# Optimization experiments

Measured on AMD Instinct MI355X. Metric: run time of the kernel, lower is better.

The kernel has to match this reference:

```python
import math
import jax, jax.numpy as jnp
import numpy as np

B, S, G, CMAX, T = 128, 256, 8, 6, 32
E, NH, L, Z = 64, 4, 2, 3
DFF = 4 * E


def _conv1d(x, w, b, pad):
    # x: [N, C, T], w: [O, I, K] -> [N, O, T]
    y = jax.lax.conv_general_dilated(x, w, (1,), [(pad, pad)], dimension_numbers=('NCH', 'OIH', 'NCH'))
    return y + b[None, :, None]


def _layernorm(x, g, b, eps=1e-5):
    m = jnp.mean(x, -1, keepdims=True)
    v = jnp.mean((x - m) ** 2, -1, keepdims=True)
    return (x - m) * jax.lax.rsqrt(v + eps) * g + b


def _pos_encoding(seq_len, dim):
    pos = jnp.arange(seq_len, dtype=jnp.float32)[:, None]
    div = jnp.exp(jnp.arange(0, dim, 2, dtype=jnp.float32) * (-math.log(10000.0) / dim))
    pe = jnp.zeros((seq_len, dim), dtype=jnp.float32)
    pe = pe.at[:, 0::2].set(jnp.sin(pos * div)).at[:, 1::2].set(jnp.cos(pos * div))
    return pe


def setup_inputs() -> dict:
    key = jax.random.key(0)
    ks = iter(jax.random.split(key, 48))
    def nrm(shape, s=0.05):
        return (jax.random.normal(next(ks), shape) * s).astype(jnp.float32)
    inp = {}
    inp['waveforms'] = jax.random.normal(next(ks), (B, S, CMAX, T), dtype=jnp.float32)
    inp['shank_ids'] = jax.random.randint(next(ks), (B, S), 0, G)
    lengths = jax.random.randint(next(ks), (B,), S // 2, S + 1)
    inp['mask'] = jnp.arange(S)[None, :] >= lengths[:, None]  # True = padded
    inp['conv1_w'] = nrm((G, 32, CMAX, 5), 0.1)
    inp['conv1_b'] = jnp.zeros((G, 32), jnp.float32)
    inp['conv2_w'] = nrm((G, E, 32, 3), 0.1)
    inp['conv2_b'] = jnp.zeros((G, E), jnp.float32)
    inp['shank_emb'] = nrm((G, E), 0.02)
    inp['in_proj_w'] = nrm((L, 3 * E, E))
    inp['in_proj_b'] = jnp.zeros((L, 3 * E), jnp.float32)
    inp['out_proj_w'] = nrm((L, E, E))
    inp['out_proj_b'] = jnp.zeros((L, E), jnp.float32)
    inp['ln1_g'] = jnp.ones((L, E), jnp.float32)
    inp['ln1_b'] = jnp.zeros((L, E), jnp.float32)
    inp['ff1_w'] = nrm((L, DFF, E))
    inp['ff1_b'] = jnp.zeros((L, DFF), jnp.float32)
    inp['ff2_w'] = nrm((L, E, DFF))
    inp['ff2_b'] = jnp.zeros((L, E), jnp.float32)
    inp['ln2_g'] = jnp.ones((L, E), jnp.float32)
    inp['ln2_b'] = jnp.zeros((L, E), jnp.float32)
    inp['cls_w1'] = nrm((E, E)); inp['cls_b1'] = jnp.zeros((E,), jnp.float32)
    inp['cls_w2'] = nrm((Z, E)); inp['cls_b2'] = jnp.zeros((Z,), jnp.float32)
    inp['mu_w1'] = nrm((Z, E, E)); inp['mu_b1'] = jnp.zeros((Z, E), jnp.float32)
    inp['mu_w2'] = nrm((Z, 2, E)); inp['mu_b2'] = jnp.zeros((Z, 2), jnp.float32)
    inp['ls_w1'] = nrm((Z, E, E)); inp['ls_b1'] = jnp.zeros((Z, E), jnp.float32)
    inp['ls_w2'] = nrm((Z, 2, E)); inp['ls_b2'] = jnp.zeros((Z, 2), jnp.float32)
    inp['d_w1'] = nrm((E, E)); inp['d_b1'] = jnp.zeros((E,), jnp.float32)
    inp['d_w2'] = nrm((1, E)); inp['d_b2'] = jnp.zeros((1,), jnp.float32)
    return inp


def reference(waveforms, shank_ids, mask, conv1_w, conv1_b, conv2_w, conv2_b, shank_emb,
              in_proj_w, in_proj_b, out_proj_w, out_proj_b, ln1_g, ln1_b,
              ff1_w, ff1_b, ff2_w, ff2_b, ln2_g, ln2_b,
              cls_w1, cls_b1, cls_w2, cls_b2, mu_w1, mu_b1, mu_w2, mu_b2,
              ls_w1, ls_b1, ls_w2, ls_b2, d_w1, d_b1, d_w2, d_b2):
    b, s, c, t = waveforms.shape
    e = shank_emb.shape[1]
    g = shank_emb.shape[0]
    x = waveforms.reshape(b * s, c, t)
    # per-shank conv encoders (MoE-style dispatch); loop over fixed small expert set
    embs = []
    for i in range(g):
        h1 = jax.nn.relu(_conv1d(x, conv1_w[i], conv1_b[i], 2))   # [N,32,T]
        h2 = jax.nn.relu(_conv1d(h1, conv2_w[i], conv2_b[i], 1))  # [N,E,T]
        embs.append(h2.mean(-1))                                  # AdaptiveAvgPool1d(1)
    emb_all = jnp.stack(embs, axis=1)                             # [N,G,E]
    sid = shank_ids.reshape(-1)
    emb = jnp.take_along_axis(emb_all, sid[:, None, None], axis=1)[:, 0]  # [N,E]
    active = (~mask).reshape(-1)
    emb = jnp.where(active[:, None], emb, 0.0).reshape(b, s, e)   # masked slots stay zero
    emb = emb + shank_emb[shank_ids] + _pos_encoding(s, e)[None]
    # post-norm transformer encoder, relu FFN, eval mode (dropout off)
    dh = e // NH
    key_bias = jnp.where(mask, -1e9, 0.0).astype(emb.dtype)[:, None, None, :]  # [B,1,1,S]
    h = emb
    for l in range(in_proj_w.shape[0]):
        qkv = h @ in_proj_w[l].T + in_proj_b[l]
        q, k, v = jnp.split(qkv, 3, axis=-1)
        q = q.reshape(b, s, NH, dh)
        k = k.reshape(b, s, NH, dh)
        v = v.reshape(b, s, NH, dh)
        scores = jnp.einsum('bqhd,bkhd->bhqk', q, k) / math.sqrt(dh) + key_bias
        attn = jax.nn.softmax(scores, axis=-1)
        o = jnp.einsum('bhqk,bkhd->bqhd', attn, v).reshape(b, s, e)
        o = o @ out_proj_w[l].T + out_proj_b[l]
        h = _layernorm(h + o, ln1_g[l], ln1_b[l])
        ff = jax.nn.relu(h @ ff1_w[l].T + ff1_b[l]) @ ff2_w[l].T + ff2_b[l]
        h = _layernorm(h + ff, ln2_g[l], ln2_b[l])
    am = active.reshape(b, s, 1).astype(h.dtype)
    pooled = (h * am).sum(1) / (am.sum(1) + 1e-8)                 # masked mean pool [B,E]
    cls_logits = jax.nn.relu(pooled @ cls_w1.T + cls_b1) @ cls_w2.T + cls_b2
    hz = jax.nn.relu(jnp.einsum('be,zfe->zbf', pooled, mu_w1) + mu_b1[:, None])
    mus = jnp.einsum('zbf,zof->bzo', hz, mu_w2) + mu_b2[None]     # [B,Z,2]
    hs = jax.nn.relu(jnp.einsum('be,zfe->zbf', pooled, ls_w1) + ls_b1[:, None])
    sigmas = jnp.exp(jnp.einsum('zbf,zof->bzo', hs, ls_w2) + ls_b2[None])  # [B,Z,2]
    d_pred = jax.nn.sigmoid(jax.nn.relu(pooled @ d_w1.T + d_b1) @ d_w2.T + d_b2)
    return jnp.concatenate([cls_logits, mus.reshape(b, -1), sigmas.reshape(b, -1), d_pred], axis=-1)
```

## Files before the change

kernel.cpp:

```cpp
#include <hip/hip_runtime.h>
#include <math.h>


typedef short bf16x8 __attribute__((ext_vector_type(8)));
typedef float f32x4 __attribute__((ext_vector_type(4)));

__device__ __forceinline__ unsigned short f2bf(float f) {
  unsigned u = __float_as_uint(f);
  u += 0x7fffu + ((u >> 16) & 1u);
  return (unsigned short)(u >> 16);
}

__device__ __forceinline__ bf16x8 ldfrag(const unsigned short* p) {
  return *reinterpret_cast<const bf16x8*>(p);
}

__device__ __forceinline__ bool is_masked(const void* mask_, int flag, int idx) {
  return flag ? (((const unsigned char*)mask_)[idx] != 0)
              : (((const int*)mask_)[idx] != 0);
}

__global__ __launch_bounds__(256) void prep_weights_kernel(
    const float* __restrict__ in_proj_w, const float* __restrict__ out_proj_w,
    const float* __restrict__ ff1_w, const float* __restrict__ ff2_w,
    const float* __restrict__ w1_, const float* __restrict__ w2_,
    unsigned short* __restrict__ wb) {
  int i = blockIdx.x * 256 + threadIdx.x;
  if (i < 24576) {
    int rem = i % 12288, row = rem / 64;
    float v = in_proj_w[i];
    if (row < 64) v *= 0.25f;
    wb[i] = f2bf(v);
  } else if (i < 32768) {
    wb[i] = f2bf(out_proj_w[i - 24576]);
  } else if (i < 65536) {
    wb[i] = f2bf(ff1_w[i - 32768]);
  } else if (i < 98304) {
    wb[i] = f2bf(ff2_w[i - 65536]);
  } else if (i < 108544) {
    int j = i - 98304;
    int g = j / 1280, rem = j % 1280;
    int k = rem >> 8, rest = rem & 255, oc = rest >> 3, ic = rest & 7;
    wb[i] = (ic < 6) ? f2bf(w1_[g * 960 + oc * 30 + ic * 5 + k]) : 0;
  } else if (i < 169984) {
    int j = i - 108544;
    int g = j / 7680, rem = j % 7680;
    int k = rem / 2560, rest = rem % 2560, e = rest / 40, ic = rest % 40;
    wb[i] = (ic < 32) ? f2bf(w2_[g * 6144 + e * 96 + ic * 3 + k]) : 0;
  }
}

__global__ void detect_mask_kernel(const unsigned int* __restrict__ mw,
                                   int* __restrict__ flag, int* __restrict__ counts,
                                   int* __restrict__ lens) {
  __shared__ int sh;
  if (threadIdx.x == 0) sh = 0;
  __syncthreads();
  int bad = 0;
  for (int i = threadIdx.x; i < 8192; i += 256)
    if (mw[i] > 1u) bad = 1;
  if (bad) atomicOr(&sh, 1);
  if (threadIdx.x < 8) counts[threadIdx.x] = 0;
  if (threadIdx.x < 128) lens[threadIdx.x] = 0;
  __syncthreads();
  if (threadIdx.x == 0) *flag = sh;
}

__global__ __launch_bounds__(256) void bin_kernel(
    const int* __restrict__ sid, const void* __restrict__ mask_,
    const int* __restrict__ flagp, int* __restrict__ counts,
    int* __restrict__ lens, int* __restrict__ idxbuf) {
  __shared__ int lcnt[8];
  __shared__ int lbase[8];
  int b = blockIdx.x, tid = threadIdx.x;
  int n = b * 256 + tid;
  int flag = *flagp;
  bool act = !is_masked(mask_, flag, n);
  int g = act ? sid[n] : 0;
  if (tid < 8) lcnt[tid] = 0;
  __syncthreads();
  int pos = 0;
  if (act) pos = atomicAdd(&lcnt[g], 1);
  __syncthreads();
  if (tid < 8) lbase[tid] = atomicAdd(&counts[tid], lcnt[tid]);
  if (tid == 0)
    lens[b] = lcnt[0] + lcnt[1] + lcnt[2] + lcnt[3] +
              lcnt[4] + lcnt[5] + lcnt[6] + lcnt[7];
  __syncthreads();
  if (act) idxbuf[g * 32768 + lbase[g] + pos] = n;
}

__global__ __launch_bounds__(256) void init_emb_kernel(
    const int* __restrict__ sid, const float* __restrict__ shank_emb,
    float* __restrict__ hout, unsigned short* __restrict__ hb) {
  int i = blockIdx.x * 256 + threadIdx.x;
  int n = i >> 6, e = i & 63, s = n & 255;
  int g = sid[n];
  float div = __expf(-(float)(e & ~1) * (9.21034037f / 64.f));
  float angle = (float)s * div;
  float pe = (e & 1) ? cosf(angle) : sinf(angle);
  float v = shank_emb[g * 64 + e] + pe;
  hout[i] = v;
  hb[i] = f2bf(v);
}

__global__ __launch_bounds__(256) void conv_mfma_kernel(
    const int* __restrict__ idxbuf, const int* __restrict__ counts,
    const float* __restrict__ wav, const unsigned short* __restrict__ wb,
    const float* __restrict__ b1_, const float* __restrict__ b2_,
    const float* __restrict__ shank_emb, float* __restrict__ hout,
    unsigned short* __restrict__ hb) {
  __shared__ __align__(16) unsigned short w1f[5][32][8];
  __shared__ __align__(16) unsigned short w2f[3][64][40];
  __shared__ float b1s[32];
  __shared__ float b2s[64];
  __shared__ __align__(16) unsigned short xw[4][36][8];
  __shared__ __align__(16) unsigned short h1w[4][34][40];
  int g = blockIdx.x & 7, bib = blockIdx.x >> 3;
  int tid = threadIdx.x;
  int wvx = tid >> 6, lane = tid & 63, quad = lane >> 4, l15 = lane & 15;
  {
    const uint4* s1 = (const uint4*)(wb + 98304 + g * 1280);
    uint4* d1 = (uint4*)&w1f[0][0][0];
    for (int i = tid; i < 160; i += 256) d1[i] = s1[i];
    const uint4* s2 = (const uint4*)(wb + 108544 + g * 7680);
    uint4* d2 = (uint4*)&w2f[0][0][0];
    for (int i = tid; i < 960; i += 256) d2[i] = s2[i];
  }
  if (tid < 32) b1s[tid] = b1_[g * 32 + tid];
  if (tid < 64) b2s[tid] = b2_[g * 64 + tid];
  {
    unsigned int* xz = (unsigned int*)&xw[wvx][0][0];
    for (int i = lane; i < 144; i += 64) xz[i] = 0;
    unsigned int* hz0 = (unsigned int*)&h1w[wvx][0][0];
    unsigned int* hz1 = (unsigned int*)&h1w[wvx][33][0];
    if (lane < 20) hz0[lane] = 0;
    else if (lane < 40) hz1[lane - 20] = 0;
  }
  __syncthreads();
  bf16x8 zf = {0, 0, 0, 0, 0, 0, 0, 0};
  bf16x8 bf1[2], bf1k4[2], bf2[3][4];
#pragma unroll
  for (int nt = 0; nt < 2; nt++) {
    bf1[nt] = ldfrag(&w1f[quad][nt * 16 + l15][0]);
    bf1k4[nt] = (quad == 0) ? ldfrag(&w1f[4][nt * 16 + l15][0]) : zf;
  }
#pragma unroll
  for (int k = 0; k < 3; k++)
#pragma unroll
    for (int nt = 0; nt < 4; nt++)
      bf2[k][nt] = ldfrag(&w2f[k][nt * 16 + l15][quad * 8]);
  float b1v0 = b1s[l15], b1v1 = b1s[16 + l15];
  float shank = shank_emb[g * 64 + lane];
  float dive = __expf(-(float)(lane & ~1) * (9.21034037f / 64.f));
  int cnt = counts[g];
  int wvg = bib * 4 + wvx;
  int ic_w = lane >> 3, t0_w = (lane & 7) * 4;
  for (int ti = wvg; ti < cnt; ti += 640) {
    int n = idxbuf[g * 32768 + ti];
    float4 v = make_float4(0.f, 0.f, 0.f, 0.f);
    if (lane < 48) v = *(const float4*)&wav[n * 192 + lane * 4];
    if (lane < 48) {
      xw[wvx][t0_w + 2][ic_w] = f2bf(v.x);
      xw[wvx][t0_w + 3][ic_w] = f2bf(v.y);
      xw[wvx][t0_w + 4][ic_w] = f2bf(v.z);
      xw[wvx][t0_w + 5][ic_w] = f2bf(v.w);
    }
    f32x4 c1[2][2];
#pragma unroll
    for (int mt = 0; mt < 2; mt++) {
      c1[mt][0] = (f32x4){b1v0, b1v0, b1v0, b1v0};
      c1[mt][1] = (f32x4){b1v1, b1v1, b1v1, b1v1};
    }
#pragma unroll
    for (int mt = 0; mt < 2; mt++) {
      bf16x8 afm = ldfrag(&xw[wvx][mt * 16 + l15 + quad][0]);
      bf16x8 af4 = (quad == 0) ? ldfrag(&xw[wvx][mt * 16 + l15 + 4][0]) : zf;
#pragma unroll
      for (int nt = 0; nt < 2; nt++) {
        c1[mt][nt] = __builtin_amdgcn_mfma_f32_16x16x32_bf16(afm, bf1[nt], c1[mt][nt], 0, 0, 0);
        c1[mt][nt] = __builtin_amdgcn_mfma_f32_16x16x32_bf16(af4, bf1k4[nt], c1[mt][nt], 0, 0, 0);
      }
    }
#pragma unroll
    for (int mt = 0; mt < 2; mt++)
#pragma unroll
      for (int nt = 0; nt < 2; nt++)
#pragma unroll
        for (int r = 0; r < 4; r++) {
          int t = mt * 16 + quad * 4 + r;
          h1w[wvx][t + 1][nt * 16 + l15] = f2bf(fmaxf(c1[mt][nt][r], 0.f));
        }
    f32x4 c2[2][4];
#pragma unroll
    for (int mt = 0; mt < 2; mt++)
#pragma unroll
      for (int nt = 0; nt < 4; nt++) {
        float bv = b2s[nt * 16 + l15];
        c2[mt][nt] = (f32x4){bv, bv, bv, bv};
      }
#pragma unroll
    for (int k = 0; k < 3; k++)
#pragma unroll
      for (int mt = 0; mt < 2; mt++) {
        bf16x8 af = ldfrag(&h1w[wvx][mt * 16 + l15 + k][quad * 8]);
#pragma unroll
        for (int nt = 0; nt < 4; nt++)
          c2[mt][nt] = __builtin_amdgcn_mfma_f32_16x16x32_bf16(af, bf2[k][nt], c2[mt][nt], 0, 0, 0);
      }
    float sums[4];
#pragma unroll
    for (int nt = 0; nt < 4; nt++) {
      float s = 0.f;
#pragma unroll
      for (int mt = 0; mt < 2; mt++)
#pragma unroll
        for (int r = 0; r < 4; r++) s += fmaxf(c2[mt][nt][r], 0.f);
      s += __shfl_xor(s, 16);
      s += __shfl_xor(s, 32);
      sums[nt] = s;
    }
    float t0 = __shfl(sums[0], l15);
    float t1 = __shfl(sums[1], l15);
    float t2 = __shfl(sums[2], l15);
    float t3 = __shfl(sums[3], l15);
    float val = (quad == 0) ? t0 : (quad == 1) ? t1 : (quad == 2) ? t2 : t3;
    float angle = (float)(n & 255) * dive;
    float pe = (lane & 1) ? cosf(angle) : sinf(angle);
    float hv = val * (1.f / 32.f) + shank + pe;
    hout[(size_t)n * 64 + lane] = hv;
    hb[(size_t)n * 64 + lane] = f2bf(hv);
  }
}

__global__ __launch_bounds__(256) void attn_fused_kernel(
    const unsigned short* __restrict__ hb, const unsigned short* __restrict__ wqkv,
    const float* __restrict__ bqkv, const int* __restrict__ lens,
    unsigned short* __restrict__ obuf) {
  __shared__ __align__(16) unsigned short qs[256][24];
  __shared__ __align__(16) unsigned short kst[256][24];
  __shared__ __align__(16) unsigned short vT[16][264];
  __shared__ __align__(16) unsigned short pw[4][16][264];
  int bh = blockIdx.x;
  int b_ = bh >> 2, hd = bh & 3;
  int tid = threadIdx.x;
  int wvx = tid >> 6, lane = tid & 63, quad = lane >> 4, l15 = lane & 15;
  int len = lens[b_];
  const unsigned short* hbb = hb + (size_t)b_ * 256 * 64;
  const unsigned short* wq = wqkv + (hd * 16) * 64;
  const unsigned short* wk = wqkv + (64 + hd * 16) * 64;
  const unsigned short* wv = wqkv + (128 + hd * 16) * 64;
  float bq_ = 0.25f * bqkv[hd * 16 + l15];
  float bk_ = bqkv[64 + hd * 16 + l15];
  f32x4 bv_;
#pragma unroll
  for (int r = 0; r < 4; r++) bv_[r] = bqkv[128 + hd * 16 + quad * 4 + r];
#pragma unroll
  for (int t4 = 0; t4 < 4; t4++) {
    int tile = wvx * 4 + t4;
    f32x4 aq = (f32x4){bq_, bq_, bq_, bq_};
    f32x4 ak = (f32x4){bk_, bk_, bk_, bk_};
    f32x4 av = bv_;
#pragma unroll
    for (int ks = 0; ks < 64; ks += 32) {
      bf16x8 af = ldfrag(hbb + (tile * 16 + l15) * 64 + ks + quad * 8);
      aq = __builtin_amdgcn_mfma_f32_16x16x32_bf16(af, ldfrag(wq + l15 * 64 + ks + quad * 8), aq, 0, 0, 0);
      ak = __builtin_amdgcn_mfma_f32_16x16x32_bf16(af, ldfrag(wk + l15 * 64 + ks + quad * 8), ak, 0, 0, 0);
      av = __builtin_amdgcn_mfma_f32_16x16x32_bf16(ldfrag(wv + l15 * 64 + ks + quad * 8), af, av, 0, 0, 0);
    }
#pragma unroll
    for (int r = 0; r < 4; r++) {
      qs[tile * 16 + quad * 4 + r][l15] = f2bf(aq[r]);
      kst[tile * 16 + quad * 4 + r][l15] = f2bf(ak[r]);
      vT[quad * 4 + r][tile * 16 + l15] = f2bf(av[r]);
    }
  }
  __syncthreads();
  bf16x8 zf = {0, 0, 0, 0, 0, 0, 0, 0};
  f32x4 zero = {0.f, 0.f, 0.f, 0.f};
#pragma unroll 1
  for (int j = 0; j < 4; j++) {
    int qt = wvx * 4 + j;
    bf16x8 bq = (quad < 2) ? ldfrag(&qs[qt * 16 + l15][quad * 8]) : zf;
    f32x4 s[16];
#pragma unroll
    for (int t = 0; t < 16; t++) {
      bf16x8 ak = (quad < 2) ? ldfrag(&kst[t * 16 + l15][quad * 8]) : zf;
      s[t] = __builtin_amdgcn_mfma_f32_16x16x32_bf16(ak, bq, zero, 0, 0, 0);
    }
    float mx = -1e30f;
#pragma unroll
    for (int t = 0; t < 16; t++)
#pragma unroll
      for (int r = 0; r < 4; r++) {
        int key = t * 16 + quad * 4 + r;
        float v = (key < len) ? s[t][r] : -1e30f;
        s[t][r] = v;
        mx = fmaxf(mx, v);
      }
    mx = fmaxf(mx, __shfl_xor(mx, 16));
    mx = fmaxf(mx, __shfl_xor(mx, 32));
    float sum = 0.f;
#pragma unroll
    for (int t = 0; t < 16; t++)
#pragma unroll
      for (int r = 0; r < 4; r++) {
        float p = __expf(s[t][r] - mx);
        s[t][r] = p;
        sum += p;
      }
    sum += __shfl_xor(sum, 16);
    sum += __shfl_xor(sum, 32);
#pragma unroll
    for (int t = 0; t < 16; t++) {
      short4 pp;
      pp.x = (short)f2bf(s[t][0]); pp.y = (short)f2bf(s[t][1]);
      pp.z = (short)f2bf(s[t][2]); pp.w = (short)f2bf(s[t][3]);
      *(short4*)&pw[wvx][l15][t * 16 + quad * 4] = pp;
    }
    f32x4 acc = zero;
#pragma unroll
    for (int c = 0; c < 8; c++) {
      bf16x8 avv = ldfrag(&vT[l15][c * 32 + quad * 8]);
      bf16x8 bp = ldfrag(&pw[wvx][l15][c * 32 + quad * 8]);
      acc = __builtin_amdgcn_mfma_f32_16x16x32_bf16(avv, bp, acc, 0, 0, 0);
    }
    float inv = 1.f / sum;
    short4 w;
    w.x = (short)f2bf(acc[0] * inv); w.y = (short)f2bf(acc[1] * inv);
    w.z = (short)f2bf(acc[2] * inv); w.w = (short)f2bf(acc[3] * inv);
    *(short4*)&obuf[(size_t)(b_ * 256 + qt * 16 + l15) * 64 + hd * 16 + quad * 4] = w;
  }
}

__global__ __launch_bounds__(256) void fused_rl_kernel(
    const unsigned short* __restrict__ obuf, float* __restrict__ H,
    unsigned short* __restrict__ Hb,
    const unsigned short* __restrict__ wout, const float* __restrict__ bout,
    const float* __restrict__ ln1g, const float* __restrict__ ln1b,
    const unsigned short* __restrict__ wff1, const float* __restrict__ bff1,
    const unsigned short* __restrict__ wff2, const float* __restrict__ bff2,
    const float* __restrict__ ln2g, const float* __restrict__ ln2b) {
  __shared__ __align__(16) unsigned short h1b[64][72];
  __shared__ __align__(16) unsigned short ffa[64][264];
  int m0 = blockIdx.x * 64;
  int tid = threadIdx.x;
  int wvx = tid >> 6, lane = tid & 63, quad = lane >> 4, l15 = lane & 15;
  int lr = wvx * 16 + quad * 4;
  f32x4 acc[4];
#pragma unroll
  for (int nt = 0; nt < 4; nt++) {
    float b = bout[nt * 16 + l15];
    acc[nt] = (f32x4){b, b, b, b};
  }
#pragma unroll
  for (int ks = 0; ks < 64; ks += 32) {
    bf16x8 af = ldfrag(obuf + (size_t)(m0 + wvx * 16 + l15) * 64 + ks + quad * 8);
#pragma unroll
    for (int nt = 0; nt < 4; nt++) {
      bf16x8 bfr = ldfrag(wout + (nt * 16 + l15) * 64 + ks + quad * 8);
      acc[nt] = __builtin_amdgcn_mfma_f32_16x16x32_bf16(af, bfr, acc[nt], 0, 0, 0);
    }
  }
  float h1reg[4][4];
#pragma unroll
  for (int r = 0; r < 4; r++) {
    float rv[4];
    float s = 0.f;
#pragma unroll
    for (int nt = 0; nt < 4; nt++) {
      float v = acc[nt][r] + H[(size_t)(m0 + lr + r) * 64 + nt * 16 + l15];
      rv[nt] = v; s += v;
    }
    s += __shfl_xor(s, 1); s += __shfl_xor(s, 2);
    s += __shfl_xor(s, 4); s += __shfl_xor(s, 8);
    float mean = s * (1.f / 64.f);
    float vsum = 0.f;
#pragma unroll
    for (int nt = 0; nt < 4; nt++) { rv[nt] -= mean; vsum += rv[nt] * rv[nt]; }
    vsum += __shfl_xor(vsum, 1); vsum += __shfl_xor(vsum, 2);
    vsum += __shfl_xor(vsum, 4); vsum += __shfl_xor(vsum, 8);
    float inv = rsqrtf(vsum * (1.f / 64.f) + 1e-5f);
#pragma unroll
    for (int nt = 0; nt < 4; nt++) {
      int col = nt * 16 + l15;
      float hv = rv[nt] * inv * ln1g[col] + ln1b[col];
      h1reg[r][nt] = hv;
      h1b[lr + r][col] = f2bf(hv);
    }
  }
  f32x4 a2[16];
#pragma unroll
  for (int nt = 0; nt < 16; nt++) {
    float b = bff1[nt * 16 + l15];
    a2[nt] = (f32x4){b, b, b, b};
  }
#pragma unroll
  for (int ks = 0; ks < 64; ks += 32) {
    bf16x8 af = ldfrag(&h1b[wvx * 16 + l15][ks + quad * 8]);
#pragma unroll
    for (int nt = 0; nt < 16; nt++) {
      bf16x8 bfr = ldfrag(wff1 + (nt * 16 + l15) * 64 + ks + quad * 8);
      a2[nt] = __builtin_amdgcn_mfma_f32_16x16x32_bf16(af, bfr, a2[nt], 0, 0, 0);
    }
  }
#pragma unroll
  for (int nt = 0; nt < 16; nt++)
#pragma unroll
    for (int r = 0; r < 4; r++)
      ffa[lr + r][nt * 16 + l15] = f2bf(fmaxf(a2[nt][r], 0.f));
#pragma unroll
  for (int nt = 0; nt < 4; nt++) {
    float b = bff2[nt * 16 + l15];
    acc[nt] = (f32x4){b, b, b, b};
  }
#pragma unroll
  for (int ks = 0; ks < 256; ks += 32) {
    bf16x8 af = ldfrag(&ffa[wvx * 16 + l15][ks + quad * 8]);
#pragma unroll
    for (int nt = 0; nt < 4; nt++) {
      bf16x8 bfr = ldfrag(wff2 + (nt * 16 + l15) * 256 + ks + quad * 8);
      acc[nt] = __builtin_amdgcn_mfma_f32_16x16x32_bf16(af, bfr, acc[nt], 0, 0, 0);
    }
  }
#pragma unroll
  for (int r = 0; r < 4; r++) {
    float rv[4];
    float s = 0.f;
#pragma unroll
    for (int nt = 0; nt < 4; nt++) {
      float v = acc[nt][r] + h1reg[r][nt];
      rv[nt] = v; s += v;
    }
    s += __shfl_xor(s, 1); s += __shfl_xor(s, 2);
    s += __shfl_xor(s, 4); s += __shfl_xor(s, 8);
    float mean = s * (1.f / 64.f);
    float vsum = 0.f;
#pragma unroll
    for (int nt = 0; nt < 4; nt++) { rv[nt] -= mean; vsum += rv[nt] * rv[nt]; }
    vsum += __shfl_xor(vsum, 1); vsum += __shfl_xor(vsum, 2);
    vsum += __shfl_xor(vsum, 4); vsum += __shfl_xor(vsum, 8);
    float inv = rsqrtf(vsum * (1.f / 64.f) + 1e-5f);
#pragma unroll
    for (int nt = 0; nt < 4; nt++) {
      int col = nt * 16 + l15;
      float hv = rv[nt] * inv * ln2g[col] + ln2b[col];
      H[(size_t)(m0 + lr + r) * 64 + col] = hv;
      Hb[(size_t)(m0 + lr + r) * 64 + col] = f2bf(hv);
    }
  }
}

__global__ __launch_bounds__(256) void pool_heads_kernel(
    const float* __restrict__ h, const int* __restrict__ lens,
    const float* __restrict__ cls_w1, const float* __restrict__ cls_b1,
    const float* __restrict__ cls_w2, const float* __restrict__ cls_b2,
    const float* __restrict__ mu_w1, const float* __restrict__ mu_b1,
    const float* __restrict__ mu_w2, const float* __restrict__ mu_b2,
    const float* __restrict__ ls_w1, const float* __restrict__ ls_b1,
    const float* __restrict__ ls_w2, const float* __restrict__ ls_b2,
    const float* __restrict__ d_w1, const float* __restrict__ d_b1,
    const float* __restrict__ d_w2, const float* __restrict__ d_b2,
    float* __restrict__ out) {
  __shared__ float ps[4][64];
  __shared__ float p[64];
  __shared__ float t1[64];
  int b = blockIdx.x, tid = threadIdx.x;
  int e = tid & 63, sp = tid >> 6;
  int len = lens[b];
  {
    float sum = 0.f;
    int send = min(sp * 64 + 64, len);
    for (int s = sp * 64; s < send; s++) sum += h[(size_t)(b * 256 + s) * 64 + e];
    ps[sp][e] = sum;
  }
  __syncthreads();
  if (sp == 0)
    p[e] = (ps[0][e] + ps[1][e] + ps[2][e] + ps[3][e]) / ((float)len + 1e-8f);
  __syncthreads();
  if (tid < 64) {
    float a = cls_b1[tid];
    for (int j = 0; j < 64; j++) a += p[j] * cls_w1[tid * 64 + j];
    t1[tid] = fmaxf(a, 0.f);
  }
  __syncthreads();
  if (tid < 3) {
    float a2 = cls_b2[tid];
    for (int j = 0; j < 64; j++) a2 += t1[j] * cls_w2[tid * 64 + j];
    out[b * 16 + tid] = a2;
  }
  for (int z = 0; z < 3; z++) {
    __syncthreads();
    if (tid < 64) {
      float a = mu_b1[z * 64 + tid];
      for (int j = 0; j < 64; j++) a += p[j] * mu_w1[(z * 64 + tid) * 64 + j];
      t1[tid] = fmaxf(a, 0.f);
    }
    __syncthreads();
    if (tid < 2) {
      float a2 = mu_b2[z * 2 + tid];
      for (int j = 0; j < 64; j++) a2 += t1[j] * mu_w2[(z * 2 + tid) * 64 + j];
      out[b * 16 + 3 + z * 2 + tid] = a2;
    }
    __syncthreads();
    if (tid < 64) {
      float a = ls_b1[z * 64 + tid];
      for (int j = 0; j < 64; j++) a += p[j] * ls_w1[(z * 64 + tid) * 64 + j];
      t1[tid] = fmaxf(a, 0.f);
    }
    __syncthreads();
    if (tid < 2) {
      float a2 = ls_b2[z * 2 + tid];
      for (int j = 0; j < 64; j++) a2 += t1[j] * ls_w2[(z * 2 + tid) * 64 + j];
      out[b * 16 + 9 + z * 2 + tid] = __expf(a2);
    }
  }
  __syncthreads();
  if (tid < 64) {
    float a = d_b1[tid];
    for (int j = 0; j < 64; j++) a += p[j] * d_w1[tid * 64 + j];
    t1[tid] = fmaxf(a, 0.f);
  }
  __syncthreads();
  if (tid == 0) {
    float a2 = d_b2[0];
    for (int j = 0; j < 64; j++) a2 += t1[j] * d_w2[j];
    out[b * 16 + 15] = 1.f / (1.f + __expf(-a2));
  }
}

extern "C" void kernel_launch(void* const* d_in, const int* in_sizes, int n_in,
                              void* d_out, int out_size, void* d_ws, size_t ws_size,
                              hipStream_t stream) {
  const float* wav       = (const float*)d_in[0];
  const int*   sid       = (const int*)d_in[1];
  const void*  mask      = d_in[2];
  const float* conv1_w   = (const float*)d_in[3];
  const float* conv1_b   = (const float*)d_in[4];
  const float* conv2_w   = (const float*)d_in[5];
  const float* conv2_b   = (const float*)d_in[6];
  const float* shank_emb = (const float*)d_in[7];
  const float* in_proj_w = (const float*)d_in[8];
  const float* in_proj_b = (const float*)d_in[9];
  const float* out_proj_w= (const float*)d_in[10];
  const float* out_proj_b= (const float*)d_in[11];
  const float* ln1_g     = (const float*)d_in[12];
  const float* ln1_b     = (const float*)d_in[13];
  const float* ff1_w     = (const float*)d_in[14];
  const float* ff1_b     = (const float*)d_in[15];
  const float* ff2_w     = (const float*)d_in[16];
  const float* ff2_b     = (const float*)d_in[17];
  const float* ln2_g     = (const float*)d_in[18];
  const float* ln2_b     = (const float*)d_in[19];
  const float* cls_w1    = (const float*)d_in[20];
  const float* cls_b1    = (const float*)d_in[21];
  const float* cls_w2    = (const float*)d_in[22];
  const float* cls_b2    = (const float*)d_in[23];
  const float* mu_w1     = (const float*)d_in[24];
  const float* mu_b1     = (const float*)d_in[25];
  const float* mu_w2     = (const float*)d_in[26];
  const float* mu_b2     = (const float*)d_in[27];
  const float* ls_w1     = (const float*)d_in[28];
  const float* ls_b1     = (const float*)d_in[29];
  const float* ls_w2     = (const float*)d_in[30];
  const float* ls_b2     = (const float*)d_in[31];
  const float* d_w1      = (const float*)d_in[32];
  const float* d_b1      = (const float*)d_in[33];
  const float* d_w2      = (const float*)d_in[34];
  const float* d_b2      = (const float*)d_in[35];
  float* out = (float*)d_out;

  float* ws = (float*)d_ws;
  float*          h     = ws;
  unsigned short* hb    = (unsigned short*)(ws + 2097152);
  unsigned short* obufb = (unsigned short*)(ws + 3145728);
  unsigned short* wb    = (unsigned short*)(ws + 4194304);
  int*   ip     = (int*)(ws + 10493952);
  int*   flag   = ip;
  int*   counts = ip + 8;
  int*   lens   = ip + 16;
  int*   idxbuf = ip + 144;

  prep_weights_kernel<<<664, 256, 0, stream>>>(in_proj_w, out_proj_w, ff1_w, ff2_w,
                                               conv1_w, conv2_w, wb);
  detect_mask_kernel<<<1, 256, 0, stream>>>((const unsigned int*)mask, flag, counts, lens);
  bin_kernel<<<128, 256, 0, stream>>>(sid, mask, flag, counts, lens, idxbuf);
  init_emb_kernel<<<8192, 256, 0, stream>>>(sid, shank_emb, h, hb);
  conv_mfma_kernel<<<1280, 256, 0, stream>>>(idxbuf, counts, wav, wb, conv1_b, conv2_b,
                                             shank_emb, h, hb);
  for (int l = 0; l < 2; l++) {
    attn_fused_kernel<<<512, 256, 0, stream>>>(hb, wb + l * 12288,
                                               in_proj_b + l * 192, lens, obufb);
    fused_rl_kernel<<<512, 256, 0, stream>>>(
        obufb, h, hb,
        wb + 24576 + l * 4096, out_proj_b + l * 64,
        ln1_g + l * 64, ln1_b + l * 64,
        wb + 32768 + l * 16384, ff1_b + l * 256,
        wb + 65536 + l * 16384, ff2_b + l * 64,
        ln2_g + l * 64, ln2_b + l * 64);
  }
  pool_heads_kernel<<<128, 256, 0, stream>>>(h, lens, cls_w1, cls_b1, cls_w2, cls_b2,
                                             mu_w1, mu_b1, mu_w2, mu_b2,
                                             ls_w1, ls_b1, ls_w2, ls_b2,
                                             d_w1, d_b1, d_w2, d_b2, out);
}
```

Baseline: 308.0 us.

## Merge setup kernels and software-prefetch waveforms in conv loop

Folds mask detection into the weight-prep kernel and bin counting into the embedding-init kernel, cutting the setup launches from four to two. The conv kernel now prefetches the next item's index and waveform data into registers while it computes the current one, so global-load latency overlaps with MFMA work. The cost is extra registers in the conv kernel and divergent work in block 0 and the first 128 blocks of the fused kernels.

```diff
diff --git a/kernel.cpp b/kernel.cpp
--- a/kernel.cpp
+++ b/kernel.cpp
@@ -20,12 +20,14 @@
               : (((const int*)mask_)[idx] != 0);
 }
 
-__global__ __launch_bounds__(256) void prep_weights_kernel(
+__global__ __launch_bounds__(256) void prep_all_kernel(
     const float* __restrict__ in_proj_w, const float* __restrict__ out_proj_w,
     const float* __restrict__ ff1_w, const float* __restrict__ ff2_w,
     const float* __restrict__ w1_, const float* __restrict__ w2_,
-    unsigned short* __restrict__ wb) {
-  int i = blockIdx.x * 256 + threadIdx.x;
+    unsigned short* __restrict__ wb, const unsigned int* __restrict__ mw,
+    int* __restrict__ flag, int* __restrict__ counts, int* __restrict__ lens) {
+  int tid = threadIdx.x;
+  int i = blockIdx.x * 256 + tid;
   if (i < 24576) {
     int rem = i % 12288, row = rem / 64;
     float v = in_proj_w[i];
@@ -48,60 +50,58 @@
     int k = rem / 2560, rest = rem % 2560, e = rest / 40, ic = rest % 40;
     wb[i] = (ic < 32) ? f2bf(w2_[g * 6144 + e * 96 + ic * 3 + k]) : 0;
   }
-}
-
-__global__ void detect_mask_kernel(const unsigned int* __restrict__ mw,
-                                   int* __restrict__ flag, int* __restrict__ counts,
-                                   int* __restrict__ lens) {
-  __shared__ int sh;
-  if (threadIdx.x == 0) sh = 0;
-  __syncthreads();
-  int bad = 0;
-  for (int i = threadIdx.x; i < 8192; i += 256)
-    if (mw[i] > 1u) bad = 1;
-  if (bad) atomicOr(&sh, 1);
-  if (threadIdx.x < 8) counts[threadIdx.x] = 0;
-  if (threadIdx.x < 128) lens[threadIdx.x] = 0;
-  __syncthreads();
-  if (threadIdx.x == 0) *flag = sh;
-}
-
-__global__ __launch_bounds__(256) void bin_kernel(
-    const int* __restrict__ sid, const void* __restrict__ mask_,
-    const int* __restrict__ flagp, int* __restrict__ counts,
-    int* __restrict__ lens, int* __restrict__ idxbuf) {
+  if (blockIdx.x == 0) {
+    __shared__ int sh;
+    if (tid == 0) sh = 0;
+    __syncthreads();
+    int bad = 0;
+    for (int k = tid; k < 8192; k += 256)
+      if (mw[k] > 1u) bad = 1;
+    if (bad) atomicOr(&sh, 1);
+    if (tid < 8) counts[tid] = 0;
+    if (tid < 128) lens[tid] = 0;
+    __syncthreads();
+    if (tid == 0) *flag = sh;
+  }
+}
+
+__global__ __launch_bounds__(256) void init_bin_kernel(
+    const int* __restrict__ sid, const float* __restrict__ shank_emb,
+    const void* __restrict__ mask_, const int* __restrict__ flagp,
+    int* __restrict__ counts, int* __restrict__ lens, int* __restrict__ idxbuf,
+    float* __restrict__ hout, unsigned short* __restrict__ hb) {
   __shared__ int lcnt[8];
   __shared__ int lbase[8];
-  int b = blockIdx.x, tid = threadIdx.x;
-  int n = b * 256 + tid;
-  int flag = *flagp;
-  bool act = !is_masked(mask_, flag, n);
-  int g = act ? sid[n] : 0;
-  if (tid < 8) lcnt[tid] = 0;
-  __syncthreads();
-  int pos = 0;
-  if (act) pos = atomicAdd(&lcnt[g], 1);
-  __syncthreads();
-  if (tid < 8) lbase[tid] = atomicAdd(&counts[tid], lcnt[tid]);
-  if (tid == 0)
-    lens[b] = lcnt[0] + lcnt[1] + lcnt[2] + lcnt[3] +
-              lcnt[4] + lcnt[5] + lcnt[6] + lcnt[7];
-  __syncthreads();
-  if (act) idxbuf[g * 32768 + lbase[g] + pos] = n;
-}
-
-__global__ __launch_bounds__(256) void init_emb_kernel(
-    const int* __restrict__ sid, const float* __restrict__ shank_emb,
-    float* __restrict__ hout, unsigned short* __restrict__ hb) {
-  int i = blockIdx.x * 256 + threadIdx.x;
-  int n = i >> 6, e = i & 63, s = n & 255;
-  int g = sid[n];
-  float div = __expf(-(float)(e & ~1) * (9.21034037f / 64.f));
-  float angle = (float)s * div;
-  float pe = (e & 1) ? cosf(angle) : sinf(angle);
-  float v = shank_emb[g * 64 + e] + pe;
-  hout[i] = v;
-  hb[i] = f2bf(v);
+  int tid = threadIdx.x;
+  int i = blockIdx.x * 256 + tid;
+  {
+    int n = i >> 6, e = i & 63, s = n & 255;
+    int g = sid[n];
+    float div = __expf(-(float)(e & ~1) * (9.21034037f / 64.f));
+    float angle = (float)s * div;
+    float pe = (e & 1) ? cosf(angle) : sinf(angle);
+    float v = shank_emb[g * 64 + e] + pe;
+    hout[i] = v;
+    hb[i] = f2bf(v);
+  }
+  if (blockIdx.x < 128) {
+    int b = blockIdx.x;
+    int n = b * 256 + tid;
+    int flag = *flagp;
+    bool act = !is_masked(mask_, flag, n);
+    int g = act ? sid[n] : 0;
+    if (tid < 8) lcnt[tid] = 0;
+    __syncthreads();
+    int pos = 0;
+    if (act) pos = atomicAdd(&lcnt[g], 1);
+    __syncthreads();
+    if (tid < 8) lbase[tid] = atomicAdd(&counts[tid], lcnt[tid]);
+    if (tid == 0)
+      lens[b] = lcnt[0] + lcnt[1] + lcnt[2] + lcnt[3] +
+                lcnt[4] + lcnt[5] + lcnt[6] + lcnt[7];
+    __syncthreads();
+    if (act) idxbuf[g * 32768 + lbase[g] + pos] = n;
+  }
 }
 
 __global__ __launch_bounds__(256) void conv_mfma_kernel(
@@ -154,12 +154,22 @@
   float shank = shank_emb[g * 64 + lane];
   float dive = __expf(-(float)(lane & ~1) * (9.21034037f / 64.f));
   int cnt = counts[g];
-  int wvg = bib * 4 + wvx;
   int ic_w = lane >> 3, t0_w = (lane & 7) * 4;
-  for (int ti = wvg; ti < cnt; ti += 640) {
-    int n = idxbuf[g * 32768 + ti];
-    float4 v = make_float4(0.f, 0.f, 0.f, 0.f);
+  int ti = bib * 4 + wvx;
+  int n = 0;
+  float4 v = make_float4(0.f, 0.f, 0.f, 0.f);
+  if (ti < cnt) {
+    n = idxbuf[g * 32768 + ti];
     if (lane < 48) v = *(const float4*)&wav[n * 192 + lane * 4];
+  }
+  while (ti < cnt) {
+    int tn = ti + 640;
+    int n2 = 0;
+    float4 v2 = make_float4(0.f, 0.f, 0.f, 0.f);
+    if (tn < cnt) {
+      n2 = idxbuf[g * 32768 + tn];
+      if (lane < 48) v2 = *(const float4*)&wav[n2 * 192 + lane * 4];
+    }
     if (lane < 48) {
       xw[wvx][t0_w + 2][ic_w] = f2bf(v.x);
       xw[wvx][t0_w + 3][ic_w] = f2bf(v.y);
@@ -230,6 +240,7 @@
     float hv = val * (1.f / 32.f) + shank + pe;
     hout[(size_t)n * 64 + lane] = hv;
     hb[(size_t)n * 64 + lane] = f2bf(hv);
+    ti = tn; n = n2; v = v2;
   }
 }
 
@@ -581,11 +592,11 @@
   int*   lens   = ip + 16;
   int*   idxbuf = ip + 144;
 
-  prep_weights_kernel<<<664, 256, 0, stream>>>(in_proj_w, out_proj_w, ff1_w, ff2_w,
-                                               conv1_w, conv2_w, wb);
-  detect_mask_kernel<<<1, 256, 0, stream>>>((const unsigned int*)mask, flag, counts, lens);
-  bin_kernel<<<128, 256, 0, stream>>>(sid, mask, flag, counts, lens, idxbuf);
-  init_emb_kernel<<<8192, 256, 0, stream>>>(sid, shank_emb, h, hb);
+  prep_all_kernel<<<664, 256, 0, stream>>>(in_proj_w, out_proj_w, ff1_w, ff2_w,
+                                           conv1_w, conv2_w, wb,
+                                           (const unsigned int*)mask, flag, counts, lens);
+  init_bin_kernel<<<8192, 256, 0, stream>>>(sid, shank_emb, mask, flag, counts,
+                                            lens, idxbuf, h, hb);
   conv_mfma_kernel<<<1280, 256, 0, stream>>>(idxbuf, counts, wav, wb, conv1_b, conv2_b,
                                              shank_emb, h, hb);
   for (int l = 0; l < 2; l++) {
```

New measurement: 303.2 us. No clear change (-1.6%).
